# Performance work log

Hardware: AMD Instinct MI355X
Metric: run time of the kernel (lower is better)

Reference implementation:

```python
import jax, jax.numpy as jnp
import numpy as np

MAX_AREA_WIDTH = 3  # from init_kwargs


def _window_vals(val, width, merge):
    """Multi-scale forward window sums: for each w in 1..width, sum val[t:t+w]
    over the seq axis, concatenated along the seq axis (total length
    width*L - width*(width-1)/2). Equivalent to the torch recurrence."""
    B, H, L, D = val.shape
    csum = jnp.concatenate(
        [jnp.zeros((B, H, 1, D), val.dtype), jnp.cumsum(val, axis=2)], axis=2)
    parts = []
    for i in range(width):
        w = i + 1
        s = csum[:, :, w:, :] - csum[:, :, :L - w + 1, :]  # [B,H,L-i,D]
        if merge == 'mean':
            s = s / jnp.asarray(w, val.dtype)
        parts.append(s)
    return jnp.concatenate(parts, axis=2)


def _window_masks(mask, width, zero_pad):
    parts = [mask[:, :, :, i:] for i in range(width)]
    m = jnp.concatenate(parts, axis=-1)  # [B,H,L,L']
    if zero_pad:
        m = m.at[:, :, 0, :].set(0)
    return m


def setup_inputs() -> dict:
    key = jax.random.key(0)
    kq, kk, kv = jax.random.split(key, 3)
    B, H, L, D = 8, 8, 512, 64
    q = jax.random.normal(kq, (B, H, L, D), jnp.float32)
    k = jax.random.normal(kk, (B, H, L, D), jnp.float32)
    v = jax.random.normal(kv, (B, H, L, D), jnp.float32)
    # causal attention mask, as used in pykt knowledge-tracing models
    mask = jnp.broadcast_to(jnp.tril(jnp.ones((L, L), jnp.int32)), (B, H, L, L))
    return {"q": q, "k": k, "v": v, "d_k": 64, "mask": mask, "zero_pad": 1}


def reference(q, k, v, d_k, mask, zero_pad):
    W = MAX_AREA_WIDTH
    k_area = _window_vals(k, W, 'mean')   # [B,H,L',D]
    v_area = _window_vals(v, W, 'sum')    # [B,H,L',D]
    m = _window_masks(mask, W, zero_pad)  # [B,H,L,L']
    scores = jnp.einsum('bhqd,bhkd->bhqk', q, k_area) / jnp.sqrt(
        jnp.asarray(d_k, jnp.float32))
    scores = jnp.where(m == 0, jnp.asarray(-1e32, scores.dtype), scores)
    attn = jax.nn.softmax(scores, axis=-1)  # dropout omitted (eval / p=0)
    return jnp.einsum('bhqk,bhkd->bhqd', attn, v_area)
```

## Files before the change

kernel.cpp:

```cpp
#include <hip/hip_runtime.h>


#define LSEQ 512
#define DDIM 64
#define BK 64
#define SPB 88
#define SSW 68

typedef __attribute__((ext_vector_type(8))) short bf8_t;
typedef __attribute__((ext_vector_type(4))) float f32x4;

__device__ __forceinline__ unsigned short f2bf(float f) {
  union { float f; unsigned u; } v; v.f = f;
  unsigned u = v.u;
  unsigned r = u + 0x7fffu + ((u >> 16) & 1u);
  return (unsigned short)(r >> 16);
}
__device__ __forceinline__ float bf2f(unsigned short h) {
  union { unsigned u; float f; } v; v.u = ((unsigned)h) << 16; return v.f;
}
__device__ __forceinline__ unsigned pk2(float a, float b) {
  return (unsigned)f2bf(a) | ((unsigned)f2bf(b) << 16);
}
__device__ __forceinline__ float ex2(float x) {
  float r; asm("v_exp_f32 %0, %1" : "=v"(r) : "v"(x)); return r;
}

__global__ __launch_bounds__(256)
void prep_kernel(const float* __restrict__ qg, const float* __restrict__ kg,
                 const float* __restrict__ vg,
                 unsigned short* __restrict__ vt,
                 unsigned short* __restrict__ qbf,
                 unsigned short* __restrict__ kbf,
                 float* __restrict__ outg) {
  const int bid = blockIdx.x, tid = threadIdx.x;
  if (bid < 512) {
    const int bh = bid >> 3, oct = bid & 7;
    const float* vb = vg + (size_t)bh * LSEQ * DDIM;
    unsigned short* vo = vt + (size_t)bh * DDIM * LSEQ;
#pragma unroll
    for (int it = 0; it < 4; ++it) {
      int item = tid + it * 256;
      int d = item & 63, tq = item >> 6;
      int t = oct * 64 + tq * 4;
      ushort4 o;
      o.x = f2bf(vb[(t + 0) * DDIM + d]);
      o.y = f2bf(vb[(t + 1) * DDIM + d]);
      o.z = f2bf(vb[(t + 2) * DDIM + d]);
      o.w = f2bf(vb[(t + 3) * DDIM + d]);
      *(ushort4*)&vo[(size_t)d * LSEQ + t] = o;
    }
  } else if (bid < 1536) {
    const bool isq = bid < 1024;
    const float4* src = (const float4*)(isq ? qg : kg);
    ushort4* dst = (ushort4*)(isq ? qbf : kbf);
    const float s = isq ? 0.125f : 1.0f;
    const int blk = bid & 511;
#pragma unroll
    for (int it = 0; it < 4; ++it) {
      int f = blk * 1024 + it * 256 + tid;
      float4 x = src[f];
      ushort4 o;
      o.x = f2bf(x.x * s); o.y = f2bf(x.y * s);
      o.z = f2bf(x.z * s); o.w = f2bf(x.w * s);
      dst[f] = o;
    }
  } else {
    __shared__ float4 red[256];
    const int bh = bid - 1536;
    const float4* vb4 = (const float4*)(vg + (size_t)bh * LSEQ * DDIM);
    const int d4 = tid & 15, rg = tid >> 4;
    float4 acc = make_float4(0.f, 0.f, 0.f, 0.f);
    for (int t = rg; t < LSEQ; t += 16) {
      float c = (t == 0 || t == LSEQ - 1) ? 3.f
              : (t == 1 || t == LSEQ - 2) ? 5.f : 6.f;
      float4 x = vb4[t * 16 + d4];
      acc.x += c * x.x; acc.y += c * x.y; acc.z += c * x.z; acc.w += c * x.w;
    }
    red[rg * 16 + d4] = acc;
    __syncthreads();
    if (rg == 0) {
      float4 sum = make_float4(0.f, 0.f, 0.f, 0.f);
#pragma unroll
      for (int g = 0; g < 16; ++g) {
        float4 x = red[g * 16 + d4];
        sum.x += x.x; sum.y += x.y; sum.z += x.z; sum.w += x.w;
      }
      const float inv = 1.0f / 1533.0f;
      sum.x *= inv; sum.y *= inv; sum.z *= inv; sum.w *= inv;
      ((float4*)(outg + (size_t)bh * LSEQ * DDIM))[d4] = sum;
    }
  }
}

__global__ __launch_bounds__(64, 4)
void area_attn_kernel(const unsigned short* __restrict__ qbf,
                      const unsigned short* __restrict__ kbf,
                      const unsigned short* __restrict__ vtg,
                      float* __restrict__ outg) {
  __shared__ __align__(16) float Ss[16][SSW];
  __shared__ __align__(16) unsigned short Ps[16 * SPB];

  const int bid = blockIdx.x;
  const int bh = bid >> 5, qt = bid & 31;
  const int q0 = qt * 16;
  const int lane = threadIdx.x;
  const int lc = lane & 15, lg = lane >> 4;
  const int koff = lg * 8;
  const int pr = lane >> 2, ps = lane & 3;
  const int ec0 = ps * 16;
  const float L2E = 1.44269504088896341f;

  const unsigned short* qb = qbf + (size_t)bh * LSEQ * DDIM;
  const unsigned short* kb = kbf + (size_t)bh * LSEQ * DDIM;
  const unsigned short* vtb = vtg + (size_t)bh * DDIM * LSEQ;

  const bf8_t qa0 = *(const bf8_t*)&qb[(size_t)(q0 + lc) * DDIM + koff];
  const bf8_t qa1 = *(const bf8_t*)&qb[(size_t)(q0 + lc) * DDIM + 32 + koff];

  f32x4 oacc[4];
#pragma unroll
  for (int nt = 0; nt < 4; ++nt) oacc[nt] = (f32x4){0.f, 0.f, 0.f, 0.f};
  float m_run = -3.0e38f, l_run = 0.f;
  float alphav = 0.f;

  const int ntiles = (qt >> 2) + 1;
  for (int kt = 0; kt < ntiles; ++kt) {
    const int t0 = kt * BK;

    if (ps == 0) {
      if (kt == 0) { Ss[pr][64] = -1.0e30f; Ss[pr][65] = -1.0e30f; }
      else         { Ss[pr][64] = Ss[pr][62]; Ss[pr][65] = Ss[pr][63]; }
    }

#pragma unroll
    for (int nt = 0; nt < 4; ++nt) {
      const size_t kr = (size_t)(t0 + nt * 16 + lc) * DDIM;
      bf8_t kf0 = *(const bf8_t*)&kb[kr + koff];
      bf8_t kf1 = *(const bf8_t*)&kb[kr + 32 + koff];
      f32x4 acc = (f32x4){0.f, 0.f, 0.f, 0.f};
      acc = __builtin_amdgcn_mfma_f32_16x16x32_bf16(qa0, kf0, acc, 0, 0, 0);
      acc = __builtin_amdgcn_mfma_f32_16x16x32_bf16(qa1, kf1, acc, 0, 0, 0);
#pragma unroll
      for (int r = 0; r < 4; ++r)
        Ss[4 * lg + r][nt * 16 + lc] = acc[r];
    }

    {
      const int vmax = q0 + pr - t0;
      float pm1, pm2;
      if (ps == 0) { pm1 = Ss[pr][65] * L2E; pm2 = Ss[pr][64] * L2E; }
      else         { pm1 = Ss[pr][ec0 - 1] * L2E; pm2 = Ss[pr][ec0 - 2] * L2E; }

      float sv[16];
      *(float4*)&sv[0]  = *(const float4*)&Ss[pr][ec0];
      *(float4*)&sv[4]  = *(const float4*)&Ss[pr][ec0 + 4];
      *(float4*)&sv[8]  = *(const float4*)&Ss[pr][ec0 + 8];
      *(float4*)&sv[12] = *(const float4*)&Ss[pr][ec0 + 12];
#pragma unroll
      for (int k = 0; k < 16; ++k) sv[k] *= L2E;

      float mloc = -3.0e38f;
      {
        float a1 = pm1, a2 = pm2;
#pragma unroll
        for (int k = 0; k < 16; ++k) {
          float s0 = sv[k];
          float t = a1 + s0;
          float mm = fmaxf(s0, fmaxf(0.5f * t, (1.0f / 3.0f) * (a2 + t)));
          if (ec0 + k <= vmax) mloc = fmaxf(mloc, mm);
          a2 = a1; a1 = s0;
        }
      }
      mloc = fmaxf(mloc, __shfl_xor(mloc, 1));
      mloc = fmaxf(mloc, __shfl_xor(mloc, 2));
      const float m_new = fmaxf(m_run, mloc);
      alphav = ex2(m_run - m_new);
      m_run = m_new;
      l_run *= alphav;

      float cf[18];
#pragma unroll
      for (int k = 0; k < 18; ++k) cf[k] = 0.f;
      float ladd = 0.f;
      {
        float a1 = pm1, a2 = pm2;
#pragma unroll
        for (int k = 0; k < 16; ++k) {
          float s0 = sv[k];
          bool vld = (ec0 + k) <= vmax;
          float t = a1 + s0;
          float p1 = vld ? ex2(s0 - m_new) : 0.f;
          float p2 = vld ? ex2(0.5f * t - m_new) : 0.f;
          float p3 = vld ? ex2((1.0f / 3.0f) * (a2 + t) - m_new) : 0.f;
          float p23 = p2 + p3, p123 = p1 + p23;
          ladd += p123;
          cf[k + 2] += p123;
          cf[k + 1] += p23;
          cf[k]     += p3;
          a2 = a1; a1 = s0;
        }
      }
      ladd += __shfl_xor(ladd, 1);
      ladd += __shfl_xor(ladd, 2);
      l_run += ladd;

      float up16 = __shfl_up(cf[16], 1, 4);
      float up17 = __shfl_up(cf[17], 1, 4);
      if (ps > 0) { cf[0] += up16; cf[1] += up17; }

      const int base = pr * SPB;
      if (ps == 0) {
        *(unsigned*)&Ps[base + 64] = pk2(cf[0], cf[1]);
#pragma unroll
        for (int j = 0; j < 7; ++j)
          *(unsigned*)&Ps[base + 2 * j] = pk2(cf[2 + 2 * j], cf[3 + 2 * j]);
      } else {
        const int tcb = 16 * ps - 2;
#pragma unroll
        for (int j = 0; j < 8; ++j)
          *(unsigned*)&Ps[base + tcb + 2 * j] = pk2(cf[2 * j], cf[2 * j + 1]);
        if (ps == 3) *(unsigned*)&Ps[base + 62] = pk2(cf[16], cf[17]);
      }
    }

    {
      float av[4];
#pragma unroll
      for (int r = 0; r < 4; ++r) av[r] = __shfl(alphav, 16 * lg + 4 * r);
#pragma unroll
      for (int nt = 0; nt < 4; ++nt)
#pragma unroll
        for (int r = 0; r < 4; ++r) oacc[nt][r] *= av[r];

      bf8_t pa0 = *(const bf8_t*)&Ps[lc * SPB + koff];
      bf8_t pa1 = *(const bf8_t*)&Ps[lc * SPB + 32 + koff];
      float cm2[4], cm1[4];
#pragma unroll
      for (int r = 0; r < 4; ++r) {
        unsigned pc = *(const unsigned*)&Ps[(4 * lg + r) * SPB + 64];
        cm2[r] = bf2f((unsigned short)(pc & 0xffffu));
        cm1[r] = bf2f((unsigned short)(pc >> 16));
      }
#pragma unroll
      for (int nt = 0; nt < 4; ++nt) {
        const size_t vr = (size_t)(nt * 16 + lc) * LSEQ + t0;
        bf8_t vf0 = *(const bf8_t*)&vtb[vr + koff];
        bf8_t vf1 = *(const bf8_t*)&vtb[vr + 32 + koff];
        oacc[nt] = __builtin_amdgcn_mfma_f32_16x16x32_bf16(pa0, vf0, oacc[nt], 0, 0, 0);
        oacc[nt] = __builtin_amdgcn_mfma_f32_16x16x32_bf16(pa1, vf1, oacc[nt], 0, 0, 0);
        unsigned vc = 0;
        if (kt > 0) vc = *(const unsigned*)&vtb[vr - 2];
        float vm2 = bf2f((unsigned short)(vc & 0xffffu));
        float vm1 = bf2f((unsigned short)(vc >> 16));
#pragma unroll
        for (int r = 0; r < 4; ++r)
          oacc[nt][r] += cm2[r] * vm2 + cm1[r] * vm1;
      }
    }
  }

#pragma unroll
  for (int r = 0; r < 4; ++r) {
    float lr = __shfl(l_run, 16 * lg + 4 * r);
    int gr = q0 + 4 * lg + r;
    if (gr != 0) {
      float inv = 1.0f / lr;
#pragma unroll
      for (int nt = 0; nt < 4; ++nt)
        outg[(size_t)(bh * LSEQ + gr) * DDIM + nt * 16 + lc] = oacc[nt][r] * inv;
    }
  }
}

extern "C" void kernel_launch(void* const* d_in, const int* in_sizes, int n_in,
                              void* d_out, int out_size, void* d_ws, size_t ws_size,
                              hipStream_t stream) {
  (void)in_sizes; (void)n_in; (void)ws_size; (void)out_size;
  const float* q = (const float*)d_in[0];
  const float* k = (const float*)d_in[1];
  const float* v = (const float*)d_in[2];
  float* out = (float*)d_out;

  unsigned short* ws = (unsigned short*)d_ws;
  unsigned short* vt  = ws;
  unsigned short* qbf = ws + 2097152;
  unsigned short* kbf = ws + 2 * 2097152;

  prep_kernel<<<dim3(1600), dim3(256), 0, stream>>>(q, k, v, vt, qbf, kbf, out);
  area_attn_kernel<<<dim3(2048), dim3(64), 0, stream>>>(qbf, kbf, vt, out);
}
```

Measured before the change: 161.3 us.

## Split causal attention into per-(query-tile, key-tile) tasks with separate reduction

Replaces the per-query-tile loop over key tiles with one wave per (q-tile, k-tile) task, 9216 tasks in all, packed four to a 256-thread block. Each task computes unnormalized exp without a running max, writes partial outputs and row sums to workspace, and a new reduce kernel sums them and normalizes. This removes the causal load imbalance and serial dependency between key tiles. In exchange it adds partial-buffer traffic and an extra launch, and drops max subtraction, which can overflow exp for large scores. Boundary scores from the previous tile are now recomputed with a scalar dot product.

```diff
diff --git a/kernel.cpp b/kernel.cpp
--- a/kernel.cpp
+++ b/kernel.cpp
@@ -3,7 +3,6 @@
 
 #define LSEQ 512
 #define DDIM 64
-#define BK 64
 #define SPB 88
 #define SSW 68
 
@@ -93,18 +92,26 @@
   }
 }
 
-__global__ __launch_bounds__(64, 4)
-void area_attn_kernel(const unsigned short* __restrict__ qbf,
+__global__ __launch_bounds__(256, 4)
+void area_task_kernel(const unsigned short* __restrict__ qbf,
                       const unsigned short* __restrict__ kbf,
                       const unsigned short* __restrict__ vtg,
-                      float* __restrict__ outg) {
-  __shared__ __align__(16) float Ss[16][SSW];
-  __shared__ __align__(16) unsigned short Ps[16 * SPB];
-
-  const int bid = blockIdx.x;
-  const int bh = bid >> 5, qt = bid & 31;
-  const int q0 = qt * 16;
-  const int lane = threadIdx.x;
+                      float* __restrict__ partials) {
+  __shared__ __align__(16) float Ss[4][16][SSW];
+  __shared__ __align__(16) unsigned short Ps[4][16 * SPB];
+
+  const int w = threadIdx.x >> 6, lane = threadIdx.x & 63;
+  const int tau = blockIdx.x * 4 + w;
+  const int bh = tau / 144;
+  const int idx = tau - bh * 144;
+  int g = 0;
+  while (2 * (g + 1) * (g + 2) <= idx) ++g;
+  const int rem = idx - 2 * g * (g + 1);
+  const int dq = rem / (g + 1);
+  const int qt = 4 * g + dq;
+  const int kt = rem - dq * (g + 1);
+  const int q0 = qt * 16, t0 = kt * 64;
+
   const int lc = lane & 15, lg = lane >> 4;
   const int koff = lg * 8;
   const int pr = lane >> 2, ps = lane & 3;
@@ -118,158 +125,170 @@
   const bf8_t qa0 = *(const bf8_t*)&qb[(size_t)(q0 + lc) * DDIM + koff];
   const bf8_t qa1 = *(const bf8_t*)&qb[(size_t)(q0 + lc) * DDIM + 32 + koff];
 
+  float val = 0.f;
+  if (kt > 0) {
+    const int prr = lane >> 2, jj = (lane >> 1) & 1, hh = lane & 1;
+    const unsigned short* qrow = qb + (size_t)(q0 + prr) * DDIM + 32 * hh;
+    const unsigned short* krow = kb + (size_t)(t0 - 2 + jj) * DDIM + 32 * hh;
+#pragma unroll
+    for (int b4 = 0; b4 < 4; ++b4) {
+      bf8_t qv = *(const bf8_t*)&qrow[b4 * 8];
+      bf8_t kv = *(const bf8_t*)&krow[b4 * 8];
+#pragma unroll
+      for (int e = 0; e < 8; ++e)
+        val = fmaf(bf2f((unsigned short)qv[e]), bf2f((unsigned short)kv[e]), val);
+    }
+    val += __shfl_xor(val, 1);
+  }
+  const float ctx2 = __shfl(val, lane & ~3);
+  const float ctx1 = __shfl(val, (lane & ~3) | 2);
+
+#pragma unroll
+  for (int nt = 0; nt < 4; ++nt) {
+    const size_t kr = (size_t)(t0 + nt * 16 + lc) * DDIM;
+    bf8_t kf0 = *(const bf8_t*)&kb[kr + koff];
+    bf8_t kf1 = *(const bf8_t*)&kb[kr + 32 + koff];
+    f32x4 acc = (f32x4){0.f, 0.f, 0.f, 0.f};
+    acc = __builtin_amdgcn_mfma_f32_16x16x32_bf16(qa0, kf0, acc, 0, 0, 0);
+    acc = __builtin_amdgcn_mfma_f32_16x16x32_bf16(qa1, kf1, acc, 0, 0, 0);
+#pragma unroll
+    for (int r = 0; r < 4; ++r)
+      Ss[w][4 * lg + r][nt * 16 + lc] = acc[r];
+  }
+
+  float lrow;
+  {
+    const int vmax = q0 + pr - t0;
+    float pm1, pm2;
+    if (ps == 0) {
+      pm1 = (kt ? ctx1 : -1.0e30f) * L2E;
+      pm2 = (kt ? ctx2 : -1.0e30f) * L2E;
+    } else {
+      pm1 = Ss[w][pr][ec0 - 1] * L2E;
+      pm2 = Ss[w][pr][ec0 - 2] * L2E;
+    }
+
+    float sv[16];
+    *(float4*)&sv[0]  = *(const float4*)&Ss[w][pr][ec0];
+    *(float4*)&sv[4]  = *(const float4*)&Ss[w][pr][ec0 + 4];
+    *(float4*)&sv[8]  = *(const float4*)&Ss[w][pr][ec0 + 8];
+    *(float4*)&sv[12] = *(const float4*)&Ss[w][pr][ec0 + 12];
+#pragma unroll
+    for (int k = 0; k < 16; ++k) sv[k] *= L2E;
+
+    float cf[18];
+#pragma unroll
+    for (int k = 0; k < 18; ++k) cf[k] = 0.f;
+    float ladd = 0.f;
+    {
+      float a1 = pm1, a2 = pm2;
+#pragma unroll
+      for (int k = 0; k < 16; ++k) {
+        float s0 = sv[k];
+        bool vld = (ec0 + k) <= vmax;
+        float t = a1 + s0;
+        float p1 = vld ? ex2(s0) : 0.f;
+        float p2 = vld ? ex2(0.5f * t) : 0.f;
+        float p3 = vld ? ex2((1.0f / 3.0f) * (a2 + t)) : 0.f;
+        float p23 = p2 + p3, p123 = p1 + p23;
+        ladd += p123;
+        cf[k + 2] += p123;
+        cf[k + 1] += p23;
+        cf[k]     += p3;
+        a2 = a1; a1 = s0;
+      }
+    }
+    ladd += __shfl_xor(ladd, 1);
+    ladd += __shfl_xor(ladd, 2);
+    lrow = ladd;
+
+    float up16 = __shfl_up(cf[16], 1, 4);
+    float up17 = __shfl_up(cf[17], 1, 4);
+    if (ps > 0) { cf[0] += up16; cf[1] += up17; }
+
+    const int base = pr * SPB;
+    if (ps == 0) {
+      *(unsigned*)&Ps[w][base + 64] = pk2(cf[0], cf[1]);
+#pragma unroll
+      for (int j = 0; j < 7; ++j)
+        *(unsigned*)&Ps[w][base + 2 * j] = pk2(cf[2 + 2 * j], cf[3 + 2 * j]);
+    } else {
+      const int tcb = 16 * ps - 2;
+#pragma unroll
+      for (int j = 0; j < 8; ++j)
+        *(unsigned*)&Ps[w][base + tcb + 2 * j] = pk2(cf[2 * j], cf[2 * j + 1]);
+      if (ps == 3) *(unsigned*)&Ps[w][base + 62] = pk2(cf[16], cf[17]);
+    }
+  }
+
   f32x4 oacc[4];
 #pragma unroll
   for (int nt = 0; nt < 4; ++nt) oacc[nt] = (f32x4){0.f, 0.f, 0.f, 0.f};
-  float m_run = -3.0e38f, l_run = 0.f;
-  float alphav = 0.f;
-
-  const int ntiles = (qt >> 2) + 1;
-  for (int kt = 0; kt < ntiles; ++kt) {
-    const int t0 = kt * BK;
-
-    if (ps == 0) {
-      if (kt == 0) { Ss[pr][64] = -1.0e30f; Ss[pr][65] = -1.0e30f; }
-      else         { Ss[pr][64] = Ss[pr][62]; Ss[pr][65] = Ss[pr][63]; }
-    }
-
+  {
+    bf8_t pa0 = *(const bf8_t*)&Ps[w][lc * SPB + koff];
+    bf8_t pa1 = *(const bf8_t*)&Ps[w][lc * SPB + 32 + koff];
+    float cm2[4], cm1[4];
+#pragma unroll
+    for (int r = 0; r < 4; ++r) {
+      unsigned pc = *(const unsigned*)&Ps[w][(4 * lg + r) * SPB + 64];
+      cm2[r] = bf2f((unsigned short)(pc & 0xffffu));
+      cm1[r] = bf2f((unsigned short)(pc >> 16));
+    }
 #pragma unroll
     for (int nt = 0; nt < 4; ++nt) {
-      const size_t kr = (size_t)(t0 + nt * 16 + lc) * DDIM;
-      bf8_t kf0 = *(const bf8_t*)&kb[kr + koff];
-      bf8_t kf1 = *(const bf8_t*)&kb[kr + 32 + koff];
-      f32x4 acc = (f32x4){0.f, 0.f, 0.f, 0.f};
-      acc = __builtin_amdgcn_mfma_f32_16x16x32_bf16(qa0, kf0, acc, 0, 0, 0);
-      acc = __builtin_amdgcn_mfma_f32_16x16x32_bf16(qa1, kf1, acc, 0, 0, 0);
+      const size_t vr = (size_t)(nt * 16 + lc) * LSEQ + t0;
+      bf8_t vf0 = *(const bf8_t*)&vtb[vr + koff];
+      bf8_t vf1 = *(const bf8_t*)&vtb[vr + 32 + koff];
+      oacc[nt] = __builtin_amdgcn_mfma_f32_16x16x32_bf16(pa0, vf0, oacc[nt], 0, 0, 0);
+      oacc[nt] = __builtin_amdgcn_mfma_f32_16x16x32_bf16(pa1, vf1, oacc[nt], 0, 0, 0);
+      unsigned vc = 0;
+      if (kt > 0) vc = *(const unsigned*)&vtb[vr - 2];
+      float vm2 = bf2f((unsigned short)(vc & 0xffffu));
+      float vm1 = bf2f((unsigned short)(vc >> 16));
 #pragma unroll
       for (int r = 0; r < 4; ++r)
-        Ss[4 * lg + r][nt * 16 + lc] = acc[r];
-    }
-
-    {
-      const int vmax = q0 + pr - t0;
-      float pm1, pm2;
-      if (ps == 0) { pm1 = Ss[pr][65] * L2E; pm2 = Ss[pr][64] * L2E; }
-      else         { pm1 = Ss[pr][ec0 - 1] * L2E; pm2 = Ss[pr][ec0 - 2] * L2E; }
-
-      float sv[16];
-      *(float4*)&sv[0]  = *(const float4*)&Ss[pr][ec0];
-      *(float4*)&sv[4]  = *(const float4*)&Ss[pr][ec0 + 4];
-      *(float4*)&sv[8]  = *(const float4*)&Ss[pr][ec0 + 8];
-      *(float4*)&sv[12] = *(const float4*)&Ss[pr][ec0 + 12];
-#pragma unroll
-      for (int k = 0; k < 16; ++k) sv[k] *= L2E;
-
-      float mloc = -3.0e38f;
-      {
-        float a1 = pm1, a2 = pm2;
-#pragma unroll
-        for (int k = 0; k < 16; ++k) {
-          float s0 = sv[k];
-          float t = a1 + s0;
-          float mm = fmaxf(s0, fmaxf(0.5f * t, (1.0f / 3.0f) * (a2 + t)));
-          if (ec0 + k <= vmax) mloc = fmaxf(mloc, mm);
-          a2 = a1; a1 = s0;
-        }
-      }
-      mloc = fmaxf(mloc, __shfl_xor(mloc, 1));
-      mloc = fmaxf(mloc, __shfl_xor(mloc, 2));
-      const float m_new = fmaxf(m_run, mloc);
-      alphav = ex2(m_run - m_new);
-      m_run = m_new;
-      l_run *= alphav;
-
-      float cf[18];
-#pragma unroll
-      for (int k = 0; k < 18; ++k) cf[k] = 0.f;
-      float ladd = 0.f;
-      {
-        float a1 = pm1, a2 = pm2;
-#pragma unroll
-        for (int k = 0; k < 16; ++k) {
-          float s0 = sv[k];
-          bool vld = (ec0 + k) <= vmax;
-          float t = a1 + s0;
-          float p1 = vld ? ex2(s0 - m_new) : 0.f;
-          float p2 = vld ? ex2(0.5f * t - m_new) : 0.f;
-          float p3 = vld ? ex2((1.0f / 3.0f) * (a2 + t) - m_new) : 0.f;
-          float p23 = p2 + p3, p123 = p1 + p23;
-          ladd += p123;
-          cf[k + 2] += p123;
-          cf[k + 1] += p23;
-          cf[k]     += p3;
-          a2 = a1; a1 = s0;
-        }
-      }
-      ladd += __shfl_xor(ladd, 1);
-      ladd += __shfl_xor(ladd, 2);
-      l_run += ladd;
-
-      float up16 = __shfl_up(cf[16], 1, 4);
-      float up17 = __shfl_up(cf[17], 1, 4);
-      if (ps > 0) { cf[0] += up16; cf[1] += up17; }
-
-      const int base = pr * SPB;
-      if (ps == 0) {
-        *(unsigned*)&Ps[base + 64] = pk2(cf[0], cf[1]);
-#pragma unroll
-        for (int j = 0; j < 7; ++j)
-          *(unsigned*)&Ps[base + 2 * j] = pk2(cf[2 + 2 * j], cf[3 + 2 * j]);
-      } else {
-        const int tcb = 16 * ps - 2;
-#pragma unroll
-        for (int j = 0; j < 8; ++j)
-          *(unsigned*)&Ps[base + tcb + 2 * j] = pk2(cf[2 * j], cf[2 * j + 1]);
-        if (ps == 3) *(unsigned*)&Ps[base + 62] = pk2(cf[16], cf[17]);
-      }
-    }
-
-    {
-      float av[4];
-#pragma unroll
-      for (int r = 0; r < 4; ++r) av[r] = __shfl(alphav, 16 * lg + 4 * r);
-#pragma unroll
-      for (int nt = 0; nt < 4; ++nt)
-#pragma unroll
-        for (int r = 0; r < 4; ++r) oacc[nt][r] *= av[r];
-
-      bf8_t pa0 = *(const bf8_t*)&Ps[lc * SPB + koff];
-      bf8_t pa1 = *(const bf8_t*)&Ps[lc * SPB + 32 + koff];
-      float cm2[4], cm1[4];
-#pragma unroll
-      for (int r = 0; r < 4; ++r) {
-        unsigned pc = *(const unsigned*)&Ps[(4 * lg + r) * SPB + 64];
-        cm2[r] = bf2f((unsigned short)(pc & 0xffffu));
-        cm1[r] = bf2f((unsigned short)(pc >> 16));
-      }
-#pragma unroll
-      for (int nt = 0; nt < 4; ++nt) {
-        const size_t vr = (size_t)(nt * 16 + lc) * LSEQ + t0;
-        bf8_t vf0 = *(const bf8_t*)&vtb[vr + koff];
-        bf8_t vf1 = *(const bf8_t*)&vtb[vr + 32 + koff];
-        oacc[nt] = __builtin_amdgcn_mfma_f32_16x16x32_bf16(pa0, vf0, oacc[nt], 0, 0, 0);
-        oacc[nt] = __builtin_amdgcn_mfma_f32_16x16x32_bf16(pa1, vf1, oacc[nt], 0, 0, 0);
-        unsigned vc = 0;
-        if (kt > 0) vc = *(const unsigned*)&vtb[vr - 2];
-        float vm2 = bf2f((unsigned short)(vc & 0xffffu));
-        float vm1 = bf2f((unsigned short)(vc >> 16));
-#pragma unroll
-        for (int r = 0; r < 4; ++r)
-          oacc[nt][r] += cm2[r] * vm2 + cm1[r] * vm1;
-      }
-    }
-  }
-
-#pragma unroll
-  for (int r = 0; r < 4; ++r) {
-    float lr = __shfl(l_run, 16 * lg + 4 * r);
-    int gr = q0 + 4 * lg + r;
-    if (gr != 0) {
-      float inv = 1.0f / lr;
-#pragma unroll
-      for (int nt = 0; nt < 4; ++nt)
-        outg[(size_t)(bh * LSEQ + gr) * DDIM + nt * 16 + lc] = oacc[nt][r] * inv;
-    }
+        oacc[nt][r] += cm2[r] * vm2 + cm1[r] * vm1;
+    }
+  }
+
+  float* pb = partials + (size_t)tau * 1040;
+#pragma unroll
+  for (int nt = 0; nt < 4; ++nt)
+#pragma unroll
+    for (int r = 0; r < 4; ++r)
+      pb[(4 * lg + r) * 64 + nt * 16 + lc] = oacc[nt][r];
+  if (ps == 0) pb[1024 + pr] = lrow;
+}
+
+__global__ __launch_bounds__(256)
+void area_reduce_kernel(const float* __restrict__ partials,
+                        float* __restrict__ outg) {
+  const int w = threadIdx.x >> 6, lane = threadIdx.x & 63;
+  const int pair = blockIdx.x * 4 + w;
+  const int bh = pair >> 5, qt = pair & 31;
+  const int g = qt >> 2, n = g + 1;
+  const int start = bh * 144 + 2 * g * (g + 1) + (qt - 4 * g) * (g + 1);
+  const int row = lane >> 2, cg = lane & 3;
+
+  f32x4 a0 = {0.f,0.f,0.f,0.f}, a1 = a0, a2 = a0, a3 = a0;
+  float la = 0.f;
+  for (int t = 0; t < n; ++t) {
+    const float* pp = partials + (size_t)(start + t) * 1040;
+    const float* pr_ = pp + row * 64 + cg * 16;
+    a0 += *(const f32x4*)&pr_[0];
+    a1 += *(const f32x4*)&pr_[4];
+    a2 += *(const f32x4*)&pr_[8];
+    a3 += *(const f32x4*)&pr_[12];
+    la += pp[1024 + row];
+  }
+  const int gr = qt * 16 + row;
+  if (gr != 0) {
+    const float inv = 1.0f / la;
+    float* ob = outg + ((size_t)bh * LSEQ + gr) * DDIM + cg * 16;
+    *(f32x4*)&ob[0]  = a0 * inv;
+    *(f32x4*)&ob[4]  = a1 * inv;
+    *(f32x4*)&ob[8]  = a2 * inv;
+    *(f32x4*)&ob[12] = a3 * inv;
   }
 }
 
@@ -286,7 +305,9 @@
   unsigned short* vt  = ws;
   unsigned short* qbf = ws + 2097152;
   unsigned short* kbf = ws + 2 * 2097152;
+  float* partials = (float*)(ws + 3 * 2097152);
 
   prep_kernel<<<dim3(1600), dim3(256), 0, stream>>>(q, k, v, vt, qbf, kbf, out);
-  area_attn_kernel<<<dim3(2048), dim3(64), 0, stream>>>(qbf, kbf, vt, out);
-}
+  area_task_kernel<<<dim3(2304), dim3(256), 0, stream>>>(qbf, kbf, vt, partials);
+  area_reduce_kernel<<<dim3(512), dim3(256), 0, stream>>>(partials, out);
+}
```

Result: slower. 166.0 us (+2.9%).
